# Performance work log

Hardware: AMD Instinct MI355X
Metric: run time of the kernel (lower is better)

## Reference

```python
import jax, jax.numpy as jnp
import numpy as np

EMB = 1024
HEADS = 16

def setup_inputs() -> dict:
    key = jax.random.key(0)
    ks = jax.random.split(key, 9)
    s = 1.0 / np.sqrt(EMB)
    x = jax.random.normal(ks[0], (2, 2048, EMB), dtype=jnp.float32)
    Wq = jax.random.normal(ks[1], (EMB, EMB), dtype=jnp.float32) * s
    bq = jax.random.normal(ks[2], (EMB,), dtype=jnp.float32) * s
    Wk = jax.random.normal(ks[3], (EMB, EMB), dtype=jnp.float32) * s
    bk = jax.random.normal(ks[4], (EMB,), dtype=jnp.float32) * s
    Wv = jax.random.normal(ks[5], (EMB, EMB), dtype=jnp.float32) * s
    bv = jax.random.normal(ks[6], (EMB,), dtype=jnp.float32) * s
    Wo = jax.random.normal(ks[7], (EMB, EMB), dtype=jnp.float32) * s
    bo = jax.random.normal(ks[8], (EMB,), dtype=jnp.float32) * s
    return {"x": x, "Wq": Wq, "bq": bq, "Wk": Wk, "bk": bk, "Wv": Wv, "bv": bv, "Wo": Wo, "bo": bo}

def reference(x, Wq, bq, Wk, bk, Wv, bv, Wo, bo):
    B, N, E = x.shape
    H = HEADS
    D = E // H
    # q/k/v projections, split heads: b n (h d) -> b h n d
    def proj(W, b):
        y = jnp.einsum('bne,ef->bnf', x, W.T) + b
        return y.reshape(B, N, H, D).transpose(0, 2, 1, 3)
    q = proj(Wq, bq)
    k = proj(Wk, bk)
    v = proj(Wv, bv)
    energy = jnp.einsum('bhqd,bhkd->bhqk', q, k)
    scaling = jnp.asarray(E, x.dtype) ** 0.5  # note: sqrt(emb_size), as in source
    att = jax.nn.softmax(energy / scaling, axis=-1)
    out = jnp.einsum('bhqk,bhkd->bhqd', att, v)
    out = out.transpose(0, 2, 1, 3).reshape(B, N, E)  # b h n d -> b n (h d)
    return jnp.einsum('bne,ef->bnf', out, Wo.T) + bo
```

## Files before the change

kernel.cpp:

```cpp
#include <hip/hip_runtime.h>
#include <hip/hip_bf16.h>
#include <stdint.h>

typedef __bf16 bf16;
typedef __bf16 bf16x8 __attribute__((ext_vector_type(8)));
typedef __bf16 bf16x4 __attribute__((ext_vector_type(4)));
typedef __bf16 bf16x2 __attribute__((ext_vector_type(2)));
typedef float  f32x4  __attribute__((ext_vector_type(4)));
typedef float  f32x16 __attribute__((ext_vector_type(16)));
typedef unsigned int uint;

#define MFMA(a,b,c)   __builtin_amdgcn_mfma_f32_16x16x32_bf16((a),(b),(c),0,0,0)
#define MFMA32(a,b,c) __builtin_amdgcn_mfma_f32_32x32x16_bf16((a),(b),(c),0,0,0)
#define EXP2(x)       __builtin_amdgcn_exp2f(x)

__device__ __forceinline__ void gload_lds16(const void* g, void* lds) {
  __builtin_amdgcn_global_load_lds(
      (const __attribute__((address_space(1))) uint32_t*)g,
      (__attribute__((address_space(3))) uint32_t*)lds, 16, 0, 0);
}

__device__ __forceinline__ uint pk_bf16(float lo, float hi) {
  bf16x2 v; v[0] = (bf16)lo; v[1] = (bf16)hi;
  return __builtin_bit_cast(uint, v);
}

__global__ __launch_bounds__(256) void k_cvt(
    const float* __restrict__ x,
    const float* __restrict__ wq, const float* __restrict__ wk,
    const float* __restrict__ wv, const float* __restrict__ wo,
    bf16* __restrict__ xb, bf16* __restrict__ wqb, bf16* __restrict__ wkb,
    bf16* __restrict__ wvb, bf16* __restrict__ wob)
{
  int r = blockIdx.y;
  const float* s; bf16* d; int n;
  switch (r) {
    case 0: s = x;  d = xb;  n = 4194304; break;
    case 1: s = wq; d = wqb; n = 1048576; break;
    case 2: s = wk; d = wkb; n = 1048576; break;
    case 3: s = wv; d = wvb; n = 1048576; break;
    default: s = wo; d = wob; n = 1048576; break;
  }
  int i = (blockIdx.x * 256 + threadIdx.x) * 8;
  if (i >= n) return;
  const float4* sp = (const float4*)(s + i);
  float4 a = sp[0], b = sp[1];
  bf16x8 o;
  o[0]=(bf16)a.x; o[1]=(bf16)a.y; o[2]=(bf16)a.z; o[3]=(bf16)a.w;
  o[4]=(bf16)b.x; o[5]=(bf16)b.y; o[6]=(bf16)b.z; o[7]=(bf16)b.w;
  *(bf16x8*)(d + i) = o;
}

__global__ __launch_bounds__(256, 2) void k_gemm_qkv(
    const bf16* __restrict__ A,
    const bf16* __restrict__ Wq, const bf16* __restrict__ Wk, const bf16* __restrict__ Wv,
    const float* __restrict__ bq, const float* __restrict__ bk, const float* __restrict__ bv,
    bf16* __restrict__ Qw, bf16* __restrict__ Kw, bf16* __restrict__ Vtw)
{
  __shared__ __align__(16) char As[2][8192];
  __shared__ __align__(16) char Bs[2][8192];
  int tid = threadIdx.x;
  int wv4 = tid >> 6, l = tid & 63, lo = l & 15, hi = l >> 4;
  int mt = blockIdx.x;
  int ft = blockIdx.y;
  int wsel = ft >> 3;
  const bf16* W = (wsel == 0) ? Wq : (wsel == 1) ? Wk : Wv;
  const float* bias = (wsel == 0) ? bq : (wsel == 1) ? bk : bv;
  int f0 = (ft & 7) * 128;
  const bf16* Ab = A + (size_t)mt * 128 * 1024;
  const bf16* Wb = W + (size_t)f0 * 1024;
  int wm = wv4 >> 1, wf = wv4 & 1;
  f32x4 acc[4][4];
  #pragma unroll
  for (int i = 0; i < 4; i++)
    #pragma unroll
    for (int j = 0; j < 4; j++) acc[i][j] = (f32x4){0.f, 0.f, 0.f, 0.f};

  #define STAGEG(t, bi) {                                              \
    int k0 = (t) * 32;                                                 \
    _Pragma("unroll")                                                  \
    for (int p = 0; p < 2; p++) {                                      \
      int sp = p * 256 + tid;                                          \
      int row = sp >> 2, s = sp & 3;                                   \
      int gc = k0 + 8 * (s ^ (row & 3));                               \
      gload_lds16(Ab + (size_t)row * 1024 + gc, As[bi] + sp * 16);     \
      gload_lds16(Wb + (size_t)row * 1024 + gc, Bs[bi] + sp * 16);     \
    } }

  STAGEG(0, 0);
  for (int t = 0; t < 32; ++t) {
    __syncthreads();
    if (t < 31) STAGEG(t + 1, (t + 1) & 1);
    const char* Ac = As[t & 1];
    const char* Bc = Bs[t & 1];
    bf16x8 af[4], bfr[4];
    #pragma unroll
    for (int ms = 0; ms < 4; ms++) {
      int row = wm * 64 + ms * 16 + lo;
      af[ms] = *(const bf16x8*)(Ac + row * 64 + 16 * (hi ^ (row & 3)));
    }
    #pragma unroll
    for (int fs = 0; fs < 4; fs++) {
      int row = wf * 64 + fs * 16 + lo;
      bfr[fs] = *(const bf16x8*)(Bc + row * 64 + 16 * (hi ^ (row & 3)));
    }
    __builtin_amdgcn_s_setprio(1);
    #pragma unroll
    for (int ms = 0; ms < 4; ms++)
      #pragma unroll
      for (int fs = 0; fs < 4; fs++)
        acc[ms][fs] = MFMA(af[ms], bfr[fs], acc[ms][fs]);
    __builtin_amdgcn_s_setprio(0);
  }
  #undef STAGEG

  float bv4[4];
  #pragma unroll
  for (int fs = 0; fs < 4; fs++) bv4[fs] = bias[f0 + wf * 64 + fs * 16 + lo];
  #pragma unroll
  for (int ms = 0; ms < 4; ms++) {
    #pragma unroll
    for (int fs = 0; fs < 4; fs++) {
      int fl = f0 + wf * 64 + fs * 16 + lo;
      int h = fl >> 6, dd = fl & 63;
      #pragma unroll
      for (int r = 0; r < 4; r++) {
        int m = mt * 128 + wm * 64 + ms * 16 + hi * 4 + r;
        int b = m >> 11, n = m & 2047;
        float val = acc[ms][fs][r] + bv4[fs];
        if (wsel == 0)      Qw[(((size_t)(b * 16 + h) * 2048 + n) * 64) + dd] = (bf16)(val * 0.0450842199527801f);
        else if (wsel == 1) Kw[(((size_t)(b * 16 + h) * 2048 + n) * 64) + dd] = (bf16)val;
        else                Vtw[(((size_t)(b * 16 + h) * 64 + dd) * 2048) + n] = (bf16)val;
      }
    }
  }
}

__global__ __launch_bounds__(256, 2) void k_attn(
    const bf16* __restrict__ Q, const bf16* __restrict__ K,
    const bf16* __restrict__ Vt, bf16* __restrict__ O)
{
  __shared__ __align__(16) char Ks[2][8192];
  __shared__ __align__(16) char Vs[2][8192];
  int tid = threadIdx.x;
  int wid = tid >> 6, l = tid & 63;
  int lq = l & 31, hi1 = l >> 5;
  int qt = blockIdx.x, bh = blockIdx.y;
  int qg = qt * 128 + wid * 32 + lq;
  const bf16* Kb = K + (size_t)bh * 2048 * 64;
  const bf16* Vb = Vt + (size_t)bh * 64 * 2048;

  bf16x8 qf[4];
  const bf16* Qb = Q + ((size_t)bh * 2048 + qg) * 64 + hi1 * 8;
  #pragma unroll
  for (int c = 0; c < 4; c++) qf[c] = *(const bf16x8*)(Qb + 16 * c);

  f32x16 o0, o1, zz;
  #pragma unroll
  for (int r = 0; r < 16; r++) { zz[r] = 0.f; o0[r] = 0.f; o1[r] = 0.f; }
  float ls = 0.f;

  int srow = tid >> 3, slot = tid & 7;
  int swz = 16 * (slot ^ (srow & 7));
  int swk = lq & 7;
  uint4 k0r, k1r, v0r, v1r;
  #define STAGE(t) {                                                          \
    k0r = *(const uint4*)(Kb + (size_t)((t)*64 + srow) * 64 + slot * 8);      \
    k1r = *(const uint4*)(Kb + (size_t)((t)*64 + srow + 32) * 64 + slot * 8); \
    v0r = *(const uint4*)(Vb + (size_t)srow * 2048 + (t)*64 + slot * 8);      \
    v1r = *(const uint4*)(Vb + (size_t)(srow + 32) * 2048 + (t)*64 + slot * 8); }
  #define WRBUF(bi) {                                  \
    *(uint4*)(Ks[bi] + srow * 128 + swz)        = k0r; \
    *(uint4*)(Ks[bi] + (srow + 32) * 128 + swz) = k1r; \
    *(uint4*)(Vs[bi] + srow * 128 + swz)        = v0r; \
    *(uint4*)(Vs[bi] + (srow + 32) * 128 + swz) = v1r; }
  #define EXPSUM(S, T0, T1, T2, T3)                     \
    _Pragma("unroll")                                   \
    for (int r = 0; r < 16; r += 4) {                   \
      S[r]   = EXP2(S[r]);   T0 += S[r];                \
      S[r+1] = EXP2(S[r+1]); T1 += S[r+1];              \
      S[r+2] = EXP2(S[r+2]); T2 += S[r+2];              \
      S[r+3] = EXP2(S[r+3]); T3 += S[r+3];              \
    }
  #define PACK(dst, plo, phi)                                                \
    _Pragma("unroll")                                                        \
    for (int m = 0; m < 2; m++) {                                            \
      uint a0 = pk_bf16(plo[8*m+0], plo[8*m+1]);                             \
      uint b0 = pk_bf16(plo[8*m+4], plo[8*m+5]);                             \
      asm volatile("v_permlane32_swap_b32 %0, %1" : "+v"(a0), "+v"(b0));     \
      uint a1 = pk_bf16(plo[8*m+2], plo[8*m+3]);                             \
      uint b1 = pk_bf16(plo[8*m+6], plo[8*m+7]);                             \
      asm volatile("v_permlane32_swap_b32 %0, %1" : "+v"(a1), "+v"(b1));     \
      dst[m] = (uint4){a0, a1, b0, b1};                                      \
      uint c0 = pk_bf16(phi[8*m+0], phi[8*m+1]);                             \
      uint d0 = pk_bf16(phi[8*m+4], phi[8*m+5]);                             \
      asm volatile("v_permlane32_swap_b32 %0, %1" : "+v"(c0), "+v"(d0));     \
      uint c1 = pk_bf16(phi[8*m+2], phi[8*m+3]);                             \
      uint d1 = pk_bf16(phi[8*m+6], phi[8*m+7]);                             \
      asm volatile("v_permlane32_swap_b32 %0, %1" : "+v"(c1), "+v"(d1));     \
      dst[2+m] = (uint4){c0, c1, d0, d1};                                    \
    }

  STAGE(0);
  WRBUF(0);
  STAGE(1);

  for (int t = 0; t < 32; ++t) {
    __syncthreads();
    const char* Kc = Ks[t & 1];
    const char* Vc = Vs[t & 1];

    bf16x8 kf0[4], kf1[4];
    #pragma unroll
    for (int c = 0; c < 4; c++) {
      kf0[c] = *(const bf16x8*)(Kc + lq * 128 + 16 * ((2*c + hi1) ^ swk));
      kf1[c] = *(const bf16x8*)(Kc + (32 + lq) * 128 + 16 * ((2*c + hi1) ^ swk));
    }

    __builtin_amdgcn_s_setprio(1);
    f32x16 s0 = MFMA32(kf0[0], qf[0], zz);
    f32x16 s1 = MFMA32(kf1[0], qf[0], zz);
    #pragma unroll
    for (int c = 1; c < 4; c++) {
      s0 = MFMA32(kf0[c], qf[c], s0);
      s1 = MFMA32(kf1[c], qf[c], s1);
    }
    __builtin_amdgcn_s_setprio(0);

    float t0 = 0.f, t1 = 0.f, t2 = 0.f, t3 = 0.f;
    EXPSUM(s0, t0, t1, t2, t3);
    EXPSUM(s1, t0, t1, t2, t3);
    ls += (t0 + t1) + (t2 + t3);

    uint4 pf[4];
    PACK(pf, s0, s1);

    __builtin_amdgcn_s_setprio(1);
    #pragma unroll
    for (int c = 0; c < 4; c++) {
      bf16x8 pb = __builtin_bit_cast(bf16x8, pf[c]);
      bf16x8 vf0 = *(const bf16x8*)(Vc + lq * 128 + 16 * ((2*c + hi1) ^ swk));
      o0 = MFMA32(vf0, pb, o0);
      bf16x8 vf1 = *(const bf16x8*)(Vc + (32 + lq) * 128 + 16 * ((2*c + hi1) ^ swk));
      o1 = MFMA32(vf1, pb, o1);
    }
    __builtin_amdgcn_s_setprio(0);

    if (t < 31) {
      WRBUF((t + 1) & 1);
      if (t < 30) STAGE(t + 2);
    }
  }
  #undef STAGE
  #undef WRBUF

  float lsum = ls + __shfl_xor(ls, 32);
  float inv = 1.0f / lsum;
  int b = bh >> 4, h = bh & 15;
  bf16* Ob = O + ((size_t)(b * 2048 + qg)) * 1024 + h * 64 + hi1 * 4;
  #pragma unroll
  for (int g = 0; g < 4; g++) {
    bf16x4 w0, w1;
    #pragma unroll
    for (int j = 0; j < 4; j++) {
      w0[j] = (bf16)(o0[4*g+j] * inv);
      w1[j] = (bf16)(o1[4*g+j] * inv);
    }
    *(bf16x4*)(Ob + g * 8)      = w0;
    *(bf16x4*)(Ob + 32 + g * 8) = w1;
  }
}

__global__ __launch_bounds__(512, 1) void k_gemm_out(
    const bf16* __restrict__ A,
    const bf16* __restrict__ W,
    const float* __restrict__ bias,
    float* __restrict__ Cout)
{
  __shared__ __align__(16) char As[2][16384];
  __shared__ __align__(16) char Bs[2][16384];
  int tid = threadIdx.x;
  int wid = tid >> 6, l = tid & 63, lo = l & 15, hi = l >> 4;
  int mt = blockIdx.x;
  int f0 = blockIdx.y * 128;
  const bf16* Ab = A + (size_t)mt * 128 * 1024;
  const bf16* Wb = W + (size_t)f0 * 1024;
  int wm = wid >> 2, wf = wid & 3;
  f32x4 acc[4][2];
  #pragma unroll
  for (int i = 0; i < 4; i++)
    #pragma unroll
    for (int j = 0; j < 2; j++) acc[i][j] = (f32x4){0.f, 0.f, 0.f, 0.f};

  #define STAGEG(t, bi) {                                              \
    int k0 = (t) * 64;                                                 \
    _Pragma("unroll")                                                  \
    for (int p = 0; p < 2; p++) {                                      \
      int sp = p * 512 + tid;                                          \
      int row = sp >> 3, s = sp & 7;                                   \
      int gc = k0 + 8 * (s ^ (row & 7));                               \
      gload_lds16(Ab + (size_t)row * 1024 + gc, As[bi] + sp * 16);     \
      gload_lds16(Wb + (size_t)row * 1024 + gc, Bs[bi] + sp * 16);     \
    } }

  STAGEG(0, 0);
  for (int t = 0; t < 16; ++t) {
    __syncthreads();
    if (t < 15) STAGEG(t + 1, (t + 1) & 1);
    const char* Ac = As[t & 1];
    const char* Bc = Bs[t & 1];
    #pragma unroll
    for (int kk = 0; kk < 2; kk++) {
      bf16x8 af[4], bfr[2];
      #pragma unroll
      for (int ms = 0; ms < 4; ms++) {
        int row = wm * 64 + ms * 16 + lo;
        af[ms] = *(const bf16x8*)(Ac + row * 128 + 16 * ((kk * 4 + hi) ^ (row & 7)));
      }
      #pragma unroll
      for (int fs = 0; fs < 2; fs++) {
        int row = wf * 32 + fs * 16 + lo;
        bfr[fs] = *(const bf16x8*)(Bc + row * 128 + 16 * ((kk * 4 + hi) ^ (row & 7)));
      }
      __builtin_amdgcn_s_setprio(1);
      #pragma unroll
      for (int ms = 0; ms < 4; ms++)
        #pragma unroll
        for (int fs = 0; fs < 2; fs++)
          acc[ms][fs] = MFMA(af[ms], bfr[fs], acc[ms][fs]);
      __builtin_amdgcn_s_setprio(0);
    }
  }
  #undef STAGEG

  float bv2[2];
  #pragma unroll
  for (int fs = 0; fs < 2; fs++) bv2[fs] = bias[f0 + wf * 32 + fs * 16 + lo];
  #pragma unroll
  for (int ms = 0; ms < 4; ms++)
    #pragma unroll
    for (int fs = 0; fs < 2; fs++) {
      int f = f0 + wf * 32 + fs * 16 + lo;
      #pragma unroll
      for (int r = 0; r < 4; r++) {
        int m = mt * 128 + wm * 64 + ms * 16 + hi * 4 + r;
        Cout[(size_t)m * 1024 + f] = acc[ms][fs][r] + bv2[fs];
      }
    }
}

extern "C" void kernel_launch(void* const* d_in, const int* in_sizes, int n_in,
                              void* d_out, int out_size, void* d_ws, size_t ws_size,
                              hipStream_t stream) {
  const float* x  = (const float*)d_in[0];
  const float* Wq = (const float*)d_in[1];
  const float* bq = (const float*)d_in[2];
  const float* Wk = (const float*)d_in[3];
  const float* bk = (const float*)d_in[4];
  const float* Wv = (const float*)d_in[5];
  const float* bv = (const float*)d_in[6];
  const float* Wo = (const float*)d_in[7];
  const float* bo = (const float*)d_in[8];
  float* out = (float*)d_out;
  char* ws = (char*)d_ws;

  bf16* xb  = (bf16*)(ws);
  bf16* wqb = (bf16*)(ws + 8388608);
  bf16* wkb = (bf16*)(ws + 10485760);
  bf16* wvb = (bf16*)(ws + 12582912);
  bf16* wob = (bf16*)(ws + 14680064);
  bf16* Qw  = (bf16*)(ws + 16777216);
  bf16* Kw  = (bf16*)(ws + 25165824);
  bf16* Vtw = (bf16*)(ws + 33554432);
  bf16* Ow  = (bf16*)(ws + 41943040);

  k_cvt<<<dim3(2048, 5), 256, 0, stream>>>(x, Wq, Wk, Wv, Wo, xb, wqb, wkb, wvb, wob);
  k_gemm_qkv<<<dim3(32, 24), 256, 0, stream>>>(xb, wqb, wkb, wvb, bq, bk, bv, Qw, Kw, Vtw);
  k_attn<<<dim3(16, 32), 256, 0, stream>>>(Qw, Kw, Vtw, Ow);
  k_gemm_out<<<dim3(32, 8), 512, 0, stream>>>(Ow, wob, bo, out);
}
```

Baseline: 112.3 us.

## Remap blocks for XCD locality and vectorize GEMM epilogue stores

Block indices in the QKV, attention and output kernels are remapped so that consecutive blocks on the same XCD share the same M tile or head, aiming to improve L2 reuse. The QKV and output GEMMs swap operand roles (computing W·A^T for Q/K and the output projection) so each lane's accumulator holds consecutive feature columns, allowing packed bf16x4 and float4 stores instead of scattered scalar stores. The LDS swizzle changes to use (row>>1)&3 in the QKV kernel. The V path keeps the original orientation but now also writes packed 4-element vectors along n.

Result: faster. 106.1 us (-5.5%).

```diff
diff --git a/kernel.cpp b/kernel.cpp
--- a/kernel.cpp
+++ b/kernel.cpp
@@ -61,14 +61,18 @@
   __shared__ __align__(16) char Bs[2][8192];
   int tid = threadIdx.x;
   int wv4 = tid >> 6, l = tid & 63, lo = l & 15, hi = l >> 4;
-  int mt = blockIdx.x;
-  int ft = blockIdx.y;
+  int f = blockIdx.y * 32 + blockIdx.x;
+  int xcd = f & 7, i8 = f >> 3;
+  int mt = xcd * 4 + (i8 & 3);
+  int ft = i8 >> 2;
   int wsel = ft >> 3;
   const bf16* W = (wsel == 0) ? Wq : (wsel == 1) ? Wk : Wv;
   const float* bias = (wsel == 0) ? bq : (wsel == 1) ? bk : bv;
   int f0 = (ft & 7) * 128;
   const bf16* Ab = A + (size_t)mt * 128 * 1024;
   const bf16* Wb = W + (size_t)f0 * 1024;
+  const bf16* Pa = (wsel < 2) ? Wb : Ab;
+  const bf16* Pb = (wsel < 2) ? Ab : Wb;
   int wm = wv4 >> 1, wf = wv4 & 1;
   f32x4 acc[4][4];
   #pragma unroll
@@ -82,9 +86,9 @@
     for (int p = 0; p < 2; p++) {                                      \
       int sp = p * 256 + tid;                                          \
       int row = sp >> 2, s = sp & 3;                                   \
-      int gc = k0 + 8 * (s ^ (row & 3));                               \
-      gload_lds16(Ab + (size_t)row * 1024 + gc, As[bi] + sp * 16);     \
-      gload_lds16(Wb + (size_t)row * 1024 + gc, Bs[bi] + sp * 16);     \
+      int gc = k0 + 8 * (s ^ ((row >> 1) & 3));                        \
+      gload_lds16(Pa + (size_t)row * 1024 + gc, As[bi] + sp * 16);     \
+      gload_lds16(Pb + (size_t)row * 1024 + gc, Bs[bi] + sp * 16);     \
     } }
 
   STAGEG(0, 0);
@@ -97,12 +101,12 @@
     #pragma unroll
     for (int ms = 0; ms < 4; ms++) {
       int row = wm * 64 + ms * 16 + lo;
-      af[ms] = *(const bf16x8*)(Ac + row * 64 + 16 * (hi ^ (row & 3)));
+      af[ms] = *(const bf16x8*)(Ac + row * 64 + 16 * (hi ^ ((row >> 1) & 3)));
     }
     #pragma unroll
     for (int fs = 0; fs < 4; fs++) {
       int row = wf * 64 + fs * 16 + lo;
-      bfr[fs] = *(const bf16x8*)(Bc + row * 64 + 16 * (hi ^ (row & 3)));
+      bfr[fs] = *(const bf16x8*)(Bc + row * 64 + 16 * (hi ^ ((row >> 1) & 3)));
     }
     __builtin_amdgcn_s_setprio(1);
     #pragma unroll
@@ -114,23 +118,39 @@
   }
   #undef STAGEG
 
-  float bv4[4];
-  #pragma unroll
-  for (int fs = 0; fs < 4; fs++) bv4[fs] = bias[f0 + wf * 64 + fs * 16 + lo];
-  #pragma unroll
-  for (int ms = 0; ms < 4; ms++) {
+  if (wsel < 2) {
+    bf16* Outp = (wsel == 0) ? Qw : Kw;
+    float qs = (wsel == 0) ? 0.0450842199527801f : 1.0f;
+    #pragma unroll
+    for (int ms = 0; ms < 4; ms++) {
+      int fl = f0 + wm * 64 + ms * 16 + hi * 4;
+      int h = fl >> 6, dd = fl & 63;
+      float4 b4 = *(const float4*)(bias + fl);
+      #pragma unroll
+      for (int fs = 0; fs < 4; fs++) {
+        int m = mt * 128 + wf * 64 + fs * 16 + lo;
+        int b = m >> 11, nn = m & 2047;
+        bf16x4 w;
+        #pragma unroll
+        for (int r = 0; r < 4; r++)
+          w[r] = (bf16)((acc[ms][fs][r] + ((const float*)&b4)[r]) * qs);
+        *(bf16x4*)(Outp + (((size_t)(b * 16 + h) * 2048 + nn) * 64) + dd) = w;
+      }
+    }
+  } else {
     #pragma unroll
     for (int fs = 0; fs < 4; fs++) {
       int fl = f0 + wf * 64 + fs * 16 + lo;
       int h = fl >> 6, dd = fl & 63;
-      #pragma unroll
-      for (int r = 0; r < 4; r++) {
-        int m = mt * 128 + wm * 64 + ms * 16 + hi * 4 + r;
-        int b = m >> 11, n = m & 2047;
-        float val = acc[ms][fs][r] + bv4[fs];
-        if (wsel == 0)      Qw[(((size_t)(b * 16 + h) * 2048 + n) * 64) + dd] = (bf16)(val * 0.0450842199527801f);
-        else if (wsel == 1) Kw[(((size_t)(b * 16 + h) * 2048 + n) * 64) + dd] = (bf16)val;
-        else                Vtw[(((size_t)(b * 16 + h) * 64 + dd) * 2048) + n] = (bf16)val;
+      float bb = bias[fl];
+      #pragma unroll
+      for (int ms = 0; ms < 4; ms++) {
+        int m = mt * 128 + wm * 64 + ms * 16 + hi * 4;
+        int b = m >> 11, nn = m & 2047;
+        bf16x4 w;
+        #pragma unroll
+        for (int r = 0; r < 4; r++) w[r] = (bf16)(acc[ms][fs][r] + bb);
+        *(bf16x4*)(Vtw + (((size_t)(b * 16 + h) * 64 + dd) * 2048) + nn) = w;
       }
     }
   }
@@ -145,7 +165,10 @@
   int tid = threadIdx.x;
   int wid = tid >> 6, l = tid & 63;
   int lq = l & 31, hi1 = l >> 5;
-  int qt = blockIdx.x, bh = blockIdx.y;
+  int f = blockIdx.y * 16 + blockIdx.x;
+  int xcd = f & 7, i8 = f >> 3;
+  int bh = xcd * 4 + (i8 & 3);
+  int qt = i8 >> 2;
   int qg = qt * 128 + wid * 32 + lq;
   const bf16* Kb = K + (size_t)bh * 2048 * 64;
   const bf16* Vb = Vt + (size_t)bh * 64 * 2048;
@@ -281,16 +304,18 @@
   __shared__ __align__(16) char Bs[2][16384];
   int tid = threadIdx.x;
   int wid = tid >> 6, l = tid & 63, lo = l & 15, hi = l >> 4;
-  int mt = blockIdx.x;
-  int f0 = blockIdx.y * 128;
+  int f = blockIdx.y * 32 + blockIdx.x;
+  int xcd = f & 7, i8 = f >> 3;
+  int mt = xcd * 4 + (i8 & 3);
+  int f0 = (i8 >> 2) * 128;
   const bf16* Ab = A + (size_t)mt * 128 * 1024;
   const bf16* Wb = W + (size_t)f0 * 1024;
-  int wm = wid >> 2, wf = wid & 3;
-  f32x4 acc[4][2];
-  #pragma unroll
-  for (int i = 0; i < 4; i++)
-    #pragma unroll
-    for (int j = 0; j < 2; j++) acc[i][j] = (f32x4){0.f, 0.f, 0.f, 0.f};
+  int wm2 = wid >> 2, wf4 = wid & 3;
+  f32x4 acc[2][4];
+  #pragma unroll
+  for (int i = 0; i < 2; i++)
+    #pragma unroll
+    for (int j = 0; j < 4; j++) acc[i][j] = (f32x4){0.f, 0.f, 0.f, 0.f};
 
   #define STAGEG(t, bi) {                                              \
     int k0 = (t) * 64;                                                 \
@@ -299,8 +324,8 @@
       int sp = p * 512 + tid;                                          \
       int row = sp >> 3, s = sp & 7;                                   \
       int gc = k0 + 8 * (s ^ (row & 7));                               \
-      gload_lds16(Ab + (size_t)row * 1024 + gc, As[bi] + sp * 16);     \
-      gload_lds16(Wb + (size_t)row * 1024 + gc, Bs[bi] + sp * 16);     \
+      gload_lds16(Wb + (size_t)row * 1024 + gc, As[bi] + sp * 16);     \
+      gload_lds16(Ab + (size_t)row * 1024 + gc, Bs[bi] + sp * 16);     \
     } }
 
   STAGEG(0, 0);
@@ -311,42 +336,43 @@
     const char* Bc = Bs[t & 1];
     #pragma unroll
     for (int kk = 0; kk < 2; kk++) {
-      bf16x8 af[4], bfr[2];
-      #pragma unroll
-      for (int ms = 0; ms < 4; ms++) {
-        int row = wm * 64 + ms * 16 + lo;
-        af[ms] = *(const bf16x8*)(Ac + row * 128 + 16 * ((kk * 4 + hi) ^ (row & 7)));
+      bf16x8 wfr[2], afr[4];
+      #pragma unroll
+      for (int i = 0; i < 2; i++) {
+        int row = wf4 * 32 + i * 16 + lo;
+        wfr[i] = *(const bf16x8*)(Ac + row * 128 + 16 * ((kk * 4 + hi) ^ (row & 7)));
       }
       #pragma unroll
-      for (int fs = 0; fs < 2; fs++) {
-        int row = wf * 32 + fs * 16 + lo;
-        bfr[fs] = *(const bf16x8*)(Bc + row * 128 + 16 * ((kk * 4 + hi) ^ (row & 7)));
+      for (int j = 0; j < 4; j++) {
+        int row = wm2 * 64 + j * 16 + lo;
+        afr[j] = *(const bf16x8*)(Bc + row * 128 + 16 * ((kk * 4 + hi) ^ (row & 7)));
       }
       __builtin_amdgcn_s_setprio(1);
       #pragma unroll
-      for (int ms = 0; ms < 4; ms++)
+      for (int i = 0; i < 2; i++)
         #pragma unroll
-        for (int fs = 0; fs < 2; fs++)
-          acc[ms][fs] = MFMA(af[ms], bfr[fs], acc[ms][fs]);
+        for (int j = 0; j < 4; j++)
+          acc[i][j] = MFMA(wfr[i], afr[j], acc[i][j]);
       __builtin_amdgcn_s_setprio(0);
     }
   }
   #undef STAGEG
 
-  float bv2[2];
-  #pragma unroll
-  for (int fs = 0; fs < 2; fs++) bv2[fs] = bias[f0 + wf * 32 + fs * 16 + lo];
-  #pragma unroll
-  for (int ms = 0; ms < 4; ms++)
-    #pragma unroll
-    for (int fs = 0; fs < 2; fs++) {
-      int f = f0 + wf * 32 + fs * 16 + lo;
-      #pragma unroll
-      for (int r = 0; r < 4; r++) {
-        int m = mt * 128 + wm * 64 + ms * 16 + hi * 4 + r;
-        Cout[(size_t)m * 1024 + f] = acc[ms][fs][r] + bv2[fs];
-      }
-    }
+  #pragma unroll
+  for (int i = 0; i < 2; i++) {
+    int fl = f0 + wf4 * 32 + i * 16 + hi * 4;
+    float4 b4 = *(const float4*)(bias + fl);
+    #pragma unroll
+    for (int j = 0; j < 4; j++) {
+      int m = mt * 128 + wm2 * 64 + j * 16 + lo;
+      float4 o;
+      o.x = acc[i][j][0] + b4.x;
+      o.y = acc[i][j][1] + b4.y;
+      o.z = acc[i][j][2] + b4.z;
+      o.w = acc[i][j][3] + b4.w;
+      *(float4*)(Cout + (size_t)m * 1024 + fl) = o;
+    }
+  }
 }
 
 extern "C" void kernel_launch(void* const* d_in, const int* in_sizes, int n_in,
```
